# Optimization experiments

Hardware: AMD Instinct MI355X
Metric: run time of the kernel (lower is better)

The kernel has to match this reference:

```python
import jax, jax.numpy as jnp
import numpy as np

N = 100000   # num_nodes
E = 1600000  # num_edges (avg degree 16)
D = 64       # embed_channels
C = 16       # num_classes
EPSILON = 0.1  # AntiSymmetricConv step size (PyG default)
GAMMA = 0.1    # AntiSymmetricConv diffusion strength (PyG default)


def setup_inputs() -> dict:
    key = jax.random.key(0)
    ks = jax.random.split(key, 9)
    s = 1.0 / np.sqrt(D)
    return {
        "edge_index": jax.random.randint(ks[0], (2, E), 0, N, dtype=jnp.int32),
        "embed_w": jax.random.normal(ks[1], (N, D), dtype=jnp.float32) * 0.1,
        "W_rel": jax.random.normal(ks[2], (D, D), dtype=jnp.float32) * s,   # GraphConv lin_rel weight
        "b_rel": jax.random.normal(ks[3], (D,), dtype=jnp.float32) * s,     # GraphConv lin_rel bias
        "W_root": jax.random.normal(ks[4], (D, D), dtype=jnp.float32) * s,  # GraphConv lin_root weight (no bias)
        "W_anti": jax.random.normal(ks[5], (D, D), dtype=jnp.float32) * s,  # AntiSymmetricConv W
        "b_anti": jax.random.normal(ks[6], (D,), dtype=jnp.float32) * s,    # AntiSymmetricConv bias
        "W_lin": jax.random.normal(ks[7], (C, D), dtype=jnp.float32) * s,   # lin2 weight
        "b_lin": jax.random.normal(ks[8], (C,), dtype=jnp.float32) * s,     # lin2 bias
    }


def reference(edge_index, embed_w, W_rel, b_rel, W_root, W_anti, b_anti, W_lin, b_lin):
    x = embed_w  # [N, D] node features = embedding table
    src, dst = edge_index[0], edge_index[1]
    # phi = GraphConv with 'add' aggregation: lin_rel(sum_j x_j) + lin_root(x)
    agg = jax.ops.segment_sum(x[src], dst, num_segments=N)  # [N, D] sparse gather+scatter-add
    h = agg @ W_rel.T + b_rel + x @ W_root.T
    # antisymmetric weight: W - W^T - gamma * I
    aW = W_anti - W_anti.T - GAMMA * jnp.eye(D, dtype=x.dtype)
    h = x @ aW.T + h + b_anti
    h = jnp.tanh(h)                       # default act of AntiSymmetricConv
    x = x + EPSILON * h                   # single iteration (num_iters=1 default)
    # dropout p=0.0 -> identity
    out = jax.nn.sigmoid(x @ W_lin.T + b_lin)  # [N, C]
    return out
```

## Files before the change

### kernel.cpp

```cpp
#include <hip/hip_runtime.h>

#define DD 64
#define CC 16
#define EPSILON 0.1f
#define GAMMA 0.1f
#define BSH 6
#define BSZ 64
#define CAP 1280
#define MAXBK 2048
#define PAD 65
#define PADW 65
#define CSH 10
#define MAXNC 128
#define CPAD 16
#define CAPC 20480
#define L1CHUNK 2048
#define L1THR 512
#define NSLICE 8
#define SRTSZ 2560

typedef float v2f __attribute__((ext_vector_type(2)));

__global__ __launch_bounds__(L1THR) void bin_coarse_conv(
        const int* __restrict__ ei, int* __restrict__ gcntc,
        unsigned* __restrict__ binned_c, int E,
        const float* __restrict__ x, unsigned* __restrict__ x_q, int N,
        const float* __restrict__ Wrel, const float* __restrict__ Wroot,
        const float* __restrict__ Wanti, const float* __restrict__ brel,
        const float* __restrict__ banti,
        float* __restrict__ B_g, float* __restrict__ bc) {
    __shared__ unsigned sorted[SRTSZ];
    __shared__ unsigned char bkt[SRTSZ];
    __shared__ int hist[MAXNC], ph[MAXNC], base[MAXNC], cur[MAXNC], gbase[MAXNC];
    __shared__ int mtot;
    const int t = threadIdx.x;
    if (t < MAXNC) hist[t] = 0;
    __syncthreads();
    const int e0 = blockIdx.x * L1CHUNK;
    unsigned ent[L1CHUNK / L1THR];
    int cbk[L1CHUNK / L1THR];
#pragma unroll
    for (int i = 0; i < L1CHUNK / L1THR; ++i) {
        int e = e0 + t + L1THR * i;
        cbk[i] = -1;
        if (e < E) {
            int src = ei[e], dst = ei[E + e];
            cbk[i] = dst >> CSH;
            ent[i] = (unsigned)src | ((unsigned)(dst & ((1 << CSH) - 1)) << 17);
            atomicAdd(&hist[cbk[i]], 1);
        }
    }
    __syncthreads();
    if (t < MAXNC) { ph[t] = (hist[t] + 3) & ~3; cur[t] = ph[t]; }
    __syncthreads();
    for (int off = 1; off < MAXNC; off <<= 1) {
        int v = 0;
        if (t < MAXNC && t >= off) v = cur[t - off];
        __syncthreads();
        if (t < MAXNC) cur[t] += v;
        __syncthreads();
    }
    if (t < MAXNC) {
        base[t] = cur[t] - ph[t];
        if (t == MAXNC - 1) mtot = cur[t];
        cur[t] = base[t];
    }
    __syncthreads();
#pragma unroll
    for (int i = 0; i < L1CHUNK / L1THR; ++i)
        if (cbk[i] >= 0) {
            int pos = atomicAdd(&cur[cbk[i]], 1);
            sorted[pos] = ent[i];
            bkt[pos] = (unsigned char)cbk[i];
        }
    __syncthreads();
    if (t < MAXNC) {
        int b0 = base[t] + hist[t], b1 = base[t] + ph[t];
        for (int p = b0; p < b1; ++p) {
            sorted[p] = 0xFFFFFFFFu;
            bkt[p] = (unsigned char)t;
        }
        gbase[t] = ph[t] ? atomicAdd(&gcntc[t * CPAD], ph[t]) : 0;
    }
    __syncthreads();
    const int m = mtot;
    for (int j4 = 4 * t; j4 < m; j4 += 4 * L1THR) {
        int cb = bkt[j4];
        int gp = gbase[cb] + (j4 - base[cb]);
        if (gp + 4 <= CAPC) {
            uint4 v = *(const uint4*)&sorted[j4];
            *(uint4*)&binned_c[(size_t)cb * CAPC + gp] = v;
        }
    }
    if (blockIdx.x == 0) {
        for (int idx = t; idx < 128 * 64; idx += L1THR) {
            int k = idx >> 6, d = idx & 63;
            float v;
            if (k < 64) {
                v = Wrel[d * 64 + k];
            } else {
                int j = k - 64;
                v = Wroot[d * 64 + j] + Wanti[d * 64 + j] - Wanti[j * 64 + d];
                if (d == j) v -= GAMMA;
            }
            B_g[idx] = v;
        }
        if (t < 64) bc[t] = brel[t] + banti[t];
    }
    const float4* x4 = (const float4*)x;
    const int M = N * (DD / 4);
    const int G = gridDim.x * L1THR;
    for (int i = blockIdx.x * L1THR + t; i < M; i += G) {
        float4 a = x4[i];
        int r = __builtin_amdgcn_cvt_pk_fp8_f32(a.x, a.y, 0, false);
        r = __builtin_amdgcn_cvt_pk_fp8_f32(a.z, a.w, r, true);
        x_q[i] = (unsigned)r;
    }
}

__global__ __launch_bounds__(256) void bin_fine(
        const int* __restrict__ gcntc, const unsigned* __restrict__ binned_c,
        int* __restrict__ gcnt, unsigned* __restrict__ binned) {
    __shared__ int hist[16];
    __shared__ int hbase[16];
    const int t = threadIdx.x;
    const int c = blockIdx.x >> 3, s = blockIdx.x & (NSLICE - 1);
    int cnt = gcntc[c * CPAD];
    if (cnt > CAPC) cnt = CAPC;
    const int per = (cnt + NSLICE - 1) / NSLICE;
    const int i0 = s * per;
    int i1 = i0 + per;
    if (i1 > cnt) i1 = cnt;
    if (t < 16) hist[t] = 0;
    __syncthreads();
    const unsigned* bcp = binned_c + (size_t)c * CAPC;
    unsigned ent[10];
#pragma unroll
    for (int j = 0; j < 10; ++j) {
        int i = i0 + t + j * 256;
        ent[j] = (i < i1) ? bcp[i] : 0xFFFFFFFFu;
        if (ent[j] != 0xFFFFFFFFu) atomicAdd(&hist[ent[j] >> (17 + BSH)], 1);
    }
    __syncthreads();
    if (t < 16) {
        hbase[t] = hist[t] ? atomicAdd(&gcnt[c * 16 + t], hist[t]) : 0;
        hist[t] = 0;
    }
    __syncthreads();
#pragma unroll
    for (int j = 0; j < 10; ++j) {
        if (ent[j] != 0xFFFFFFFFu) {
            unsigned dstc = ent[j] >> 17;
            int f = dstc >> BSH;
            int pos = hbase[f] + atomicAdd(&hist[f], 1);
            if (pos < CAP)
                binned[(size_t)(c * 16 + f) * CAP + pos] =
                    (ent[j] & 0x1FFFF) | ((dstc & (BSZ - 1)) << 17);
        }
    }
}

__global__ __launch_bounds__(512, 8) void mega(
        const float* __restrict__ x, const unsigned* __restrict__ x_q,
        const int* __restrict__ gcnt, const unsigned* __restrict__ binned,
        const float* __restrict__ B_g, const float* __restrict__ bc,
        const float* __restrict__ Wlin, const float* __restrict__ blin,
        float* __restrict__ out, int N) {
    __shared__ float R0[BSZ * PAD];
    __shared__ float wl_sh[CC * PADW];
    __shared__ int csr[CAP];
    __shared__ int deg[BSZ], offs[BSZ], cur[BSZ];

    const int t = threadIdx.x;
    const int b = blockIdx.x;
    const int nb0 = b << BSH;
    int cnt = gcnt[b];
    if (cnt > CAP) cnt = CAP;
    const unsigned* bl = binned + (size_t)b * CAP;

#pragma unroll
    for (int i = 0; i < 2; ++i) {
        int idx = t + 512 * i;
        wl_sh[(idx >> 6) * PADW + (idx & 63)] = Wlin[idx];
    }
    if (t < BSZ) deg[t] = 0;
    __syncthreads();
    for (int i = t; i < cnt; i += 512) atomicAdd(&deg[bl[i] >> 17], 1);
    __syncthreads();
    if (t < BSZ) offs[t] = deg[t];
    __syncthreads();
    for (int off = 1; off < BSZ; off <<= 1) {
        int v = 0;
        if (t < BSZ && t >= off) v = offs[t - off];
        __syncthreads();
        if (t < BSZ) offs[t] += v;
        __syncthreads();
    }
    if (t < BSZ) {
        int ex = offs[t] - deg[t];
        offs[t] = ex;
        cur[t] = ex;
    }
    __syncthreads();
    for (int i = t; i < cnt; i += 512) {
        unsigned en = bl[i];
        int pos = atomicAdd(&cur[en >> 17], 1);
        csr[pos] = (int)(en & 0x1FFFF);
    }
    __syncthreads();

    {
        const int g = t >> 3, q = t & 7;
        const uint2* xq2 = (const uint2*)x_q;
        const int i0 = offs[g], dc = deg[g];
        float a[8];
#pragma unroll
        for (int r = 0; r < 8; ++r) a[r] = 0.f;
        int i = 0;
        for (; i + 8 <= dc; i += 8) {
            int s0 = csr[i0 + i + 0], s1 = csr[i0 + i + 1];
            int s2 = csr[i0 + i + 2], s3 = csr[i0 + i + 3];
            int s4 = csr[i0 + i + 4], s5 = csr[i0 + i + 5];
            int s6 = csr[i0 + i + 6], s7 = csr[i0 + i + 7];
            uint2 v0 = xq2[s0 * 8 + q];
            uint2 v1 = xq2[s1 * 8 + q];
            uint2 v2 = xq2[s2 * 8 + q];
            uint2 v3 = xq2[s3 * 8 + q];
            uint2 v4 = xq2[s4 * 8 + q];
            uint2 v5 = xq2[s5 * 8 + q];
            uint2 v6 = xq2[s6 * 8 + q];
            uint2 v7 = xq2[s7 * 8 + q];
            v2f f;
#define ACC8(v)                                                               \
            f = __builtin_amdgcn_cvt_pk_f32_fp8((v).x, false); a[0] += f.x; a[1] += f.y; \
            f = __builtin_amdgcn_cvt_pk_f32_fp8((v).x, true);  a[2] += f.x; a[3] += f.y; \
            f = __builtin_amdgcn_cvt_pk_f32_fp8((v).y, false); a[4] += f.x; a[5] += f.y; \
            f = __builtin_amdgcn_cvt_pk_f32_fp8((v).y, true);  a[6] += f.x; a[7] += f.y;
            ACC8(v0); ACC8(v1); ACC8(v2); ACC8(v3);
            ACC8(v4); ACC8(v5); ACC8(v6); ACC8(v7);
        }
        for (; i < dc; ++i) {
            int s0 = csr[i0 + i];
            uint2 v0 = xq2[s0 * 8 + q];
            v2f f;
            ACC8(v0);
#undef ACC8
        }
        float* row = &R0[g * PAD + 8 * q];
#pragma unroll
        for (int r = 0; r < 8; ++r) row[r] = a[r];
    }
    __syncthreads();

    const int nl = t & 63;
    const int dg = __builtin_amdgcn_readfirstlane(t >> 6);
    float acc[8];
#pragma unroll
    for (int j = 0; j < 8; ++j) acc[j] = 0.f;
#pragma unroll 8
    for (int k = 0; k < DD; ++k) {
        float a = R0[nl * PAD + k];
        const float* Bk = &B_g[k * DD + dg * 8];
#pragma unroll
        for (int j = 0; j < 8; ++j) acc[j] = fmaf(a, Bk[j], acc[j]);
    }
    __syncthreads();

    {
        int nn = N - nb0;
        if (nn > BSZ) nn = BSZ;
        const float4* x4 = (const float4*)x;
        for (int idx = t; idx < nn * 16; idx += 512) {
            float4 v = x4[nb0 * 16 + idx];
            float* row = &R0[(idx >> 4) * PAD + (idx & 15) * 4];
            row[0] = v.x; row[1] = v.y; row[2] = v.z; row[3] = v.w;
        }
    }
    __syncthreads();

#pragma unroll 8
    for (int k = 0; k < DD; ++k) {
        float a = R0[nl * PAD + k];
        const float* Bk = &B_g[(DD + k) * DD + dg * 8];
#pragma unroll
        for (int j = 0; j < 8; ++j) acc[j] = fmaf(a, Bk[j], acc[j]);
    }

#pragma unroll
    for (int j = 0; j < 8; ++j) {
        int d = dg * 8 + j;
        float h = acc[j] + bc[d];
        float e2 = __expf(2.0f * h);
        float th = 1.0f - 2.0f / (e2 + 1.0f);
        acc[j] = R0[nl * PAD + d] + EPSILON * th;
    }
    __syncthreads();
#pragma unroll
    for (int j = 0; j < 8; ++j) R0[nl * PAD + dg * 8 + j] = acc[j];
    __syncthreads();

    {
        const int g = t >> 3, q = t & 7;
        const int n = nb0 + g;
        if (n < N) {
            float p0 = blin[2 * q], p1 = blin[2 * q + 1];
#pragma unroll 8
            for (int d = 0; d < DD; ++d) {
                float xv = R0[g * PAD + d];
                p0 = fmaf(xv, wl_sh[(2 * q) * PADW + d], p0);
                p1 = fmaf(xv, wl_sh[(2 * q + 1) * PADW + d], p1);
            }
            float2 o;
            o.x = 1.0f / (1.0f + __expf(-p0));
            o.y = 1.0f / (1.0f + __expf(-p1));
            *(float2*)(out + (size_t)n * CC + 2 * q) = o;
        }
    }
}

extern "C" void kernel_launch(void* const* d_in, const int* in_sizes, int n_in,
                              void* d_out, int out_size, void* d_ws, size_t ws_size,
                              hipStream_t stream) {
    const int*   ei    = (const int*)d_in[0];
    const float* x     = (const float*)d_in[1];
    const float* Wrel  = (const float*)d_in[2];
    const float* brel  = (const float*)d_in[3];
    const float* Wroot = (const float*)d_in[4];
    const float* Wanti = (const float*)d_in[5];
    const float* banti = (const float*)d_in[6];
    const float* Wlin  = (const float*)d_in[7];
    const float* blin  = (const float*)d_in[8];
    float* out = (float*)d_out;

    const int E = in_sizes[0] / 2;
    const int N = in_sizes[1] / DD;
    const int NC = (N + (1 << CSH) - 1) >> CSH;

    unsigned* x_q = (unsigned*)d_ws;
    unsigned* binned_c = x_q + (size_t)N * (DD / 4);
    unsigned* binned = binned_c + (size_t)MAXNC * CAPC;
    int*   gcntc = (int*)(binned + (size_t)MAXBK * CAP);
    int*   gcnt  = gcntc + MAXNC * CPAD;
    float* B_g   = (float*)(gcnt + MAXBK);
    float* bc    = B_g + 128 * 64;

    hipMemsetAsync(gcntc, 0, (MAXNC * CPAD + MAXBK) * sizeof(int), stream);
    bin_coarse_conv<<<(E + L1CHUNK - 1) / L1CHUNK, L1THR, 0, stream>>>(
        ei, gcntc, binned_c, E, x, x_q, N,
        Wrel, Wroot, Wanti, brel, banti, B_g, bc);
    bin_fine<<<NC * NSLICE, 256, 0, stream>>>(gcntc, binned_c, gcnt, binned);
    mega<<<NC * 16, 512, 0, stream>>>(x, x_q, gcnt, binned, B_g, bc, Wlin, blin,
                                      out, N);
}
```

Measured before the change: 176.1 us.

## Replace two-level edge binning with direct global-atomic scatter into fine buckets

Drops the coarse-bin shared-memory sort and the separate fine-binning kernel. Each edge now takes a slot in its 64-node bucket with a global atomicAdd on a padded counter and writes its packed entry straight to that slot. This removes one kernel launch and a full intermediate write and read of the binned edges. The cost is 1.6M global atomics spread over about 1.6K counters, plus scattered, uncoalesced 4-byte stores in place of the earlier uint4 block stores.

```diff
diff --git a/kernel.cpp b/kernel.cpp
--- a/kernel.cpp
+++ b/kernel.cpp
@@ -10,86 +10,41 @@
 #define MAXBK 2048
 #define PAD 65
 #define PADW 65
-#define CSH 10
-#define MAXNC 128
 #define CPAD 16
-#define CAPC 20480
 #define L1CHUNK 2048
 #define L1THR 512
-#define NSLICE 8
-#define SRTSZ 2560
 
 typedef float v2f __attribute__((ext_vector_type(2)));
 
-__global__ __launch_bounds__(L1THR) void bin_coarse_conv(
-        const int* __restrict__ ei, int* __restrict__ gcntc,
-        unsigned* __restrict__ binned_c, int E,
+__global__ __launch_bounds__(L1THR) void bin_scatter_conv(
+        const int* __restrict__ ei, int* __restrict__ gcnt,
+        unsigned* __restrict__ binned, int E,
         const float* __restrict__ x, unsigned* __restrict__ x_q, int N,
         const float* __restrict__ Wrel, const float* __restrict__ Wroot,
         const float* __restrict__ Wanti, const float* __restrict__ brel,
         const float* __restrict__ banti,
         float* __restrict__ B_g, float* __restrict__ bc) {
-    __shared__ unsigned sorted[SRTSZ];
-    __shared__ unsigned char bkt[SRTSZ];
-    __shared__ int hist[MAXNC], ph[MAXNC], base[MAXNC], cur[MAXNC], gbase[MAXNC];
-    __shared__ int mtot;
     const int t = threadIdx.x;
-    if (t < MAXNC) hist[t] = 0;
-    __syncthreads();
     const int e0 = blockIdx.x * L1CHUNK;
-    unsigned ent[L1CHUNK / L1THR];
-    int cbk[L1CHUNK / L1THR];
+    int srcv[L1CHUNK / L1THR], dstv[L1CHUNK / L1THR];
 #pragma unroll
     for (int i = 0; i < L1CHUNK / L1THR; ++i) {
         int e = e0 + t + L1THR * i;
-        cbk[i] = -1;
         if (e < E) {
-            int src = ei[e], dst = ei[E + e];
-            cbk[i] = dst >> CSH;
-            ent[i] = (unsigned)src | ((unsigned)(dst & ((1 << CSH) - 1)) << 17);
-            atomicAdd(&hist[cbk[i]], 1);
-        }
-    }
-    __syncthreads();
-    if (t < MAXNC) { ph[t] = (hist[t] + 3) & ~3; cur[t] = ph[t]; }
-    __syncthreads();
-    for (int off = 1; off < MAXNC; off <<= 1) {
-        int v = 0;
-        if (t < MAXNC && t >= off) v = cur[t - off];
-        __syncthreads();
-        if (t < MAXNC) cur[t] += v;
-        __syncthreads();
-    }
-    if (t < MAXNC) {
-        base[t] = cur[t] - ph[t];
-        if (t == MAXNC - 1) mtot = cur[t];
-        cur[t] = base[t];
-    }
-    __syncthreads();
-#pragma unroll
-    for (int i = 0; i < L1CHUNK / L1THR; ++i)
-        if (cbk[i] >= 0) {
-            int pos = atomicAdd(&cur[cbk[i]], 1);
-            sorted[pos] = ent[i];
-            bkt[pos] = (unsigned char)cbk[i];
-        }
-    __syncthreads();
-    if (t < MAXNC) {
-        int b0 = base[t] + hist[t], b1 = base[t] + ph[t];
-        for (int p = b0; p < b1; ++p) {
-            sorted[p] = 0xFFFFFFFFu;
-            bkt[p] = (unsigned char)t;
-        }
-        gbase[t] = ph[t] ? atomicAdd(&gcntc[t * CPAD], ph[t]) : 0;
-    }
-    __syncthreads();
-    const int m = mtot;
-    for (int j4 = 4 * t; j4 < m; j4 += 4 * L1THR) {
-        int cb = bkt[j4];
-        int gp = gbase[cb] + (j4 - base[cb]);
-        if (gp + 4 <= CAPC) {
-            uint4 v = *(const uint4*)&sorted[j4];
-            *(uint4*)&binned_c[(size_t)cb * CAPC + gp] = v;
+            srcv[i] = ei[e];
+            dstv[i] = ei[E + e];
+        } else {
+            dstv[i] = -1;
+        }
+    }
+#pragma unroll
+    for (int i = 0; i < L1CHUNK / L1THR; ++i) {
+        if (dstv[i] >= 0) {
+            int bkt = dstv[i] >> BSH;
+            int pos = atomicAdd(&gcnt[bkt * CPAD], 1);
+            if (pos < CAP)
+                binned[(size_t)bkt * CAP + pos] =
+                    (unsigned)srcv[i] | ((unsigned)(dstv[i] & (BSZ - 1)) << 17);
         }
     }
     if (blockIdx.x == 0) {
@@ -118,48 +73,6 @@
     }
 }
 
-__global__ __launch_bounds__(256) void bin_fine(
-        const int* __restrict__ gcntc, const unsigned* __restrict__ binned_c,
-        int* __restrict__ gcnt, unsigned* __restrict__ binned) {
-    __shared__ int hist[16];
-    __shared__ int hbase[16];
-    const int t = threadIdx.x;
-    const int c = blockIdx.x >> 3, s = blockIdx.x & (NSLICE - 1);
-    int cnt = gcntc[c * CPAD];
-    if (cnt > CAPC) cnt = CAPC;
-    const int per = (cnt + NSLICE - 1) / NSLICE;
-    const int i0 = s * per;
-    int i1 = i0 + per;
-    if (i1 > cnt) i1 = cnt;
-    if (t < 16) hist[t] = 0;
-    __syncthreads();
-    const unsigned* bcp = binned_c + (size_t)c * CAPC;
-    unsigned ent[10];
-#pragma unroll
-    for (int j = 0; j < 10; ++j) {
-        int i = i0 + t + j * 256;
-        ent[j] = (i < i1) ? bcp[i] : 0xFFFFFFFFu;
-        if (ent[j] != 0xFFFFFFFFu) atomicAdd(&hist[ent[j] >> (17 + BSH)], 1);
-    }
-    __syncthreads();
-    if (t < 16) {
-        hbase[t] = hist[t] ? atomicAdd(&gcnt[c * 16 + t], hist[t]) : 0;
-        hist[t] = 0;
-    }
-    __syncthreads();
-#pragma unroll
-    for (int j = 0; j < 10; ++j) {
-        if (ent[j] != 0xFFFFFFFFu) {
-            unsigned dstc = ent[j] >> 17;
-            int f = dstc >> BSH;
-            int pos = hbase[f] + atomicAdd(&hist[f], 1);
-            if (pos < CAP)
-                binned[(size_t)(c * 16 + f) * CAP + pos] =
-                    (ent[j] & 0x1FFFF) | ((dstc & (BSZ - 1)) << 17);
-        }
-    }
-}
-
 __global__ __launch_bounds__(512, 8) void mega(
         const float* __restrict__ x, const unsigned* __restrict__ x_q,
         const int* __restrict__ gcnt, const unsigned* __restrict__ binned,
@@ -174,7 +87,7 @@
     const int t = threadIdx.x;
     const int b = blockIdx.x;
     const int nb0 = b << BSH;
-    int cnt = gcnt[b];
+    int cnt = gcnt[b * CPAD];
     if (cnt > CAP) cnt = CAP;
     const unsigned* bl = binned + (size_t)b * CAP;
 
@@ -334,21 +247,18 @@
 
     const int E = in_sizes[0] / 2;
     const int N = in_sizes[1] / DD;
-    const int NC = (N + (1 << CSH) - 1) >> CSH;
+    const int NB = (N + BSZ - 1) / BSZ;
 
     unsigned* x_q = (unsigned*)d_ws;
-    unsigned* binned_c = x_q + (size_t)N * (DD / 4);
-    unsigned* binned = binned_c + (size_t)MAXNC * CAPC;
-    int*   gcntc = (int*)(binned + (size_t)MAXBK * CAP);
-    int*   gcnt  = gcntc + MAXNC * CPAD;
-    float* B_g   = (float*)(gcnt + MAXBK);
+    unsigned* binned = x_q + (size_t)N * (DD / 4);
+    int*   gcnt  = (int*)(binned + (size_t)MAXBK * CAP);
+    float* B_g   = (float*)(gcnt + MAXBK * CPAD);
     float* bc    = B_g + 128 * 64;
 
-    hipMemsetAsync(gcntc, 0, (MAXNC * CPAD + MAXBK) * sizeof(int), stream);
-    bin_coarse_conv<<<(E + L1CHUNK - 1) / L1CHUNK, L1THR, 0, stream>>>(
-        ei, gcntc, binned_c, E, x, x_q, N,
+    hipMemsetAsync(gcnt, 0, MAXBK * CPAD * sizeof(int), stream);
+    bin_scatter_conv<<<(E + L1CHUNK - 1) / L1CHUNK, L1THR, 0, stream>>>(
+        ei, gcnt, binned, E, x, x_q, N,
         Wrel, Wroot, Wanti, brel, banti, B_g, bc);
-    bin_fine<<<NC * NSLICE, 256, 0, stream>>>(gcntc, binned_c, gcnt, binned);
-    mega<<<NC * 16, 512, 0, stream>>>(x, x_q, gcnt, binned, B_g, bc, Wlin, blin,
-                                      out, N);
+    mega<<<NB, 512, 0, stream>>>(x, x_q, gcnt, binned, B_g, bc, Wlin, blin,
+                                 out, N);
 }
```

New measurement: 226.8 us. 1.29x slower.

## Drop LDS staging sort in coarse binning; scatter edges directly to global bins

Applied to the files above, without the earlier changes.

The coarse binning kernel no longer sorts each chunk's edges in shared memory with a prefix scan, padding and vectorized uint4 flushes. Each thread now loads 4 contiguous edges with int4 reads, builds the histogram, reserves global space per bucket, and writes each entry straight to its global bin position using a shared atomic offset. This removes the scan, the multiple barriers and the LDS traffic. In exchange, global writes become scattered 4-byte stores instead of coalesced 16-byte runs, and bins are no longer padded to multiples of 4, which any downstream code assuming that padding or 0xFFFFFFFF sentinels may rely on.

```diff
diff --git a/kernel.cpp b/kernel.cpp
--- a/kernel.cpp
+++ b/kernel.cpp
@@ -17,7 +17,6 @@
 #define L1CHUNK 2048
 #define L1THR 512
 #define NSLICE 8
-#define SRTSZ 2560
 
 typedef float v2f __attribute__((ext_vector_type(2)));
 
@@ -29,67 +28,43 @@
         const float* __restrict__ Wanti, const float* __restrict__ brel,
         const float* __restrict__ banti,
         float* __restrict__ B_g, float* __restrict__ bc) {
-    __shared__ unsigned sorted[SRTSZ];
-    __shared__ unsigned char bkt[SRTSZ];
-    __shared__ int hist[MAXNC], ph[MAXNC], base[MAXNC], cur[MAXNC], gbase[MAXNC];
-    __shared__ int mtot;
+    __shared__ int hist[MAXNC], gbase[MAXNC], cur[MAXNC];
     const int t = threadIdx.x;
-    if (t < MAXNC) hist[t] = 0;
+    if (t < MAXNC) { hist[t] = 0; cur[t] = 0; }
     __syncthreads();
     const int e0 = blockIdx.x * L1CHUNK;
-    unsigned ent[L1CHUNK / L1THR];
-    int cbk[L1CHUNK / L1THR];
-#pragma unroll
-    for (int i = 0; i < L1CHUNK / L1THR; ++i) {
-        int e = e0 + t + L1THR * i;
-        cbk[i] = -1;
-        if (e < E) {
-            int src = ei[e], dst = ei[E + e];
-            cbk[i] = dst >> CSH;
-            ent[i] = (unsigned)src | ((unsigned)(dst & ((1 << CSH) - 1)) << 17);
-            atomicAdd(&hist[cbk[i]], 1);
-        }
-    }
-    __syncthreads();
-    if (t < MAXNC) { ph[t] = (hist[t] + 3) & ~3; cur[t] = ph[t]; }
-    __syncthreads();
-    for (int off = 1; off < MAXNC; off <<= 1) {
-        int v = 0;
-        if (t < MAXNC && t >= off) v = cur[t - off];
-        __syncthreads();
-        if (t < MAXNC) cur[t] += v;
-        __syncthreads();
-    }
+    int srcv[4], dstv[4];
+    const int e = e0 + 4 * t;
+    if (e + 4 <= E) {
+        int4 s4 = *(const int4*)&ei[e];
+        int4 d4 = *(const int4*)&ei[E + e];
+        srcv[0] = s4.x; srcv[1] = s4.y; srcv[2] = s4.z; srcv[3] = s4.w;
+        dstv[0] = d4.x; dstv[1] = d4.y; dstv[2] = d4.z; dstv[3] = d4.w;
+    } else {
+#pragma unroll
+        for (int i = 0; i < 4; ++i) {
+            if (e + i < E) { srcv[i] = ei[e + i]; dstv[i] = ei[E + e + i]; }
+            else dstv[i] = -1;
+        }
+    }
+#pragma unroll
+    for (int i = 0; i < 4; ++i)
+        if (dstv[i] >= 0) atomicAdd(&hist[dstv[i] >> CSH], 1);
+    __syncthreads();
     if (t < MAXNC) {
-        base[t] = cur[t] - ph[t];
-        if (t == MAXNC - 1) mtot = cur[t];
-        cur[t] = base[t];
-    }
-    __syncthreads();
-#pragma unroll
-    for (int i = 0; i < L1CHUNK / L1THR; ++i)
-        if (cbk[i] >= 0) {
-            int pos = atomicAdd(&cur[cbk[i]], 1);
-            sorted[pos] = ent[i];
-            bkt[pos] = (unsigned char)cbk[i];
-        }
-    __syncthreads();
-    if (t < MAXNC) {
-        int b0 = base[t] + hist[t], b1 = base[t] + ph[t];
-        for (int p = b0; p < b1; ++p) {
-            sorted[p] = 0xFFFFFFFFu;
-            bkt[p] = (unsigned char)t;
-        }
-        gbase[t] = ph[t] ? atomicAdd(&gcntc[t * CPAD], ph[t]) : 0;
-    }
-    __syncthreads();
-    const int m = mtot;
-    for (int j4 = 4 * t; j4 < m; j4 += 4 * L1THR) {
-        int cb = bkt[j4];
-        int gp = gbase[cb] + (j4 - base[cb]);
-        if (gp + 4 <= CAPC) {
-            uint4 v = *(const uint4*)&sorted[j4];
-            *(uint4*)&binned_c[(size_t)cb * CAPC + gp] = v;
+        int h = hist[t];
+        gbase[t] = h ? atomicAdd(&gcntc[t * CPAD], h) : 0;
+    }
+    __syncthreads();
+#pragma unroll
+    for (int i = 0; i < 4; ++i) {
+        if (dstv[i] >= 0) {
+            int b = dstv[i] >> CSH;
+            int pos = gbase[b] + atomicAdd(&cur[b], 1);
+            if (pos < CAPC)
+                binned_c[(size_t)b * CAPC + pos] =
+                    (unsigned)srcv[i] |
+                    ((unsigned)(dstv[i] & ((1 << CSH) - 1)) << 17);
         }
     }
     if (blockIdx.x == 0) {
```

Result: no change. 177.1 us (+0.6%).
